# Optimization experiments

Measured on AMD Instinct MI355X. Metric: run time of the kernel, lower is better.

The kernel has to match this reference:

```python
import jax, jax.numpy as jnp
import numpy as np


def _pairwise_sqdist(x, y):
    # x: [B, N, D], y: [B, M, D] -> P: [B, N, M] squared euclidean distances
    xx = jnp.sum(x * x, axis=-1)              # [B, N]
    yy = jnp.sum(y * y, axis=-1)              # [B, M]
    zz = jnp.einsum('bnd,bmd->bnm', x, y)     # [B, N, M]
    return xx[:, :, None] + yy[:, None, :] - 2.0 * zz


def setup_inputs() -> dict:
    key = jax.random.key(0)
    k1, k2 = jax.random.split(key)
    B, N, D = 8, 8192, 3
    preds = jax.random.normal(k1, (B, N, D), dtype=jnp.float32)
    gts = jax.random.normal(k2, (B, N, D), dtype=jnp.float32)
    return {"preds": preds, "gts": gts}


def reference(preds, gts):
    # P = batch_pairwise_dist(gts, preds): P[b, i, j] = ||gts[b,i] - preds[b,j]||^2
    P = _pairwise_sqdist(gts, preds)          # [B, N_gts, N_preds]
    loss_1 = jnp.sum(jnp.min(P, axis=1))      # min over gts points
    loss_2 = jnp.sum(jnp.min(P, axis=2))      # min over pred points
    return loss_1 + loss_2
```

## Files before the change

### kernel.cpp

```cpp
#include <hip/hip_runtime.h>

typedef _Float16 f16;
typedef f16 half8 __attribute__((ext_vector_type(8)));
typedef float f32x16 __attribute__((ext_vector_type(16)));

#define BB 8
#define NN 8192
#define SETPTS (BB * NN)
#define NPTS (2 * SETPTS)
#define TQ NPTS

__device__ __forceinline__ void gload_lds16(const void* g, void* l) {
  __builtin_amdgcn_global_load_lds(
      (const __attribute__((address_space(1))) void*)g,
      (__attribute__((address_space(3))) void*)l, 16, 0, 0);
}

__global__ __launch_bounds__(256) void chamfer_prep(
    const float* __restrict__ preds, const float* __restrict__ gts,
    float* __restrict__ yy, half8* __restrict__ Aq, half8* __restrict__ Bq) {
  int idx = blockIdx.x * 256 + threadIdx.x;
  int s = idx >> 16;
  int off = idx & (SETPTS - 1);
  const float* src = s ? gts : preds;
  float x0 = src[off * 3 + 0], x1 = src[off * 3 + 1], x2 = src[off * 3 + 2];

  f16 h0 = (f16)x0; f16 l0 = (f16)(x0 - (float)h0);
  f16 h1 = (f16)x1; f16 l1 = (f16)(x1 - (float)h1);
  f16 h2 = (f16)x2; f16 l2 = (f16)(x2 - (float)h2);

  float Y0 = -2.f * x0, Y1 = -2.f * x1, Y2 = -2.f * x2;
  f16 H0 = (f16)Y0; f16 L0 = (f16)(Y0 - (float)H0);
  f16 H1 = (f16)Y1; f16 L1 = (f16)(Y1 - (float)H1);
  f16 H2 = (f16)Y2; f16 L2 = (f16)(Y2 - (float)H2);

  float yv = x0 * x0 + x1 * x1 + x2 * x2;
  f16 yh = (f16)yv; f16 yl = (f16)(yv - (float)yh);

  f16 one = (f16)1.f, zz = (f16)0.f;
  half8 A0 = {h0, l0, h0, l0, h1, l1, h1, l1};
  half8 A1 = {h2, l2, h2, l2, one, one, zz, zz};
  half8 B0 = {H0, H0, L0, L0, H1, H1, L1, L1};
  half8 B1 = {H2, H2, L2, L2, yh, yl, zz, zz};

  Aq[idx * 2 + 0] = A0; Aq[idx * 2 + 1] = A1;
  Bq[idx * 2 + 0] = B0; Bq[idx * 2 + 1] = B1;
  yy[idx] = yv;
}

template <int R>
__global__ __launch_bounds__(256, 4) void chamfer_mfma(
    const half8* __restrict__ Aq, const half8* __restrict__ Bq,
    float* __restrict__ partial) {
  constexpr int NSTEP = NN / R / 32;
  constexpr int CH = 16;
  constexpr int NCH = NSTEP / CH;
  __shared__ __align__(16) char lds[2][CH * 1024];

  int bi = blockIdx.x;
  int xcd = bi & 7;
  int idx = bi >> 3;
  int panel = xcd * 2 + (idx & 1);
  int dir = panel >> 3;
  int b = panel & 7;
  int sub = idx >> 1;
  int qb = sub & 31;
  int r = sub >> 5;

  int tid = threadIdx.x;
  int w = tid >> 6;
  int l = tid & 63;
  int l31 = l & 31;
  int lh = l >> 5;

  const half8* Qp =
      Aq + ((size_t)(dir * BB + b) * NN + qb * 256 + w * 64) * 2;
  half8 q0 = Qp[l31 * 2 + lh];
  half8 q1 = Qp[(32 + l31) * 2 + lh];

  const char* gpanel = (const char*)(Bq + ((size_t)((1 - dir) * BB + b) * NN +
                                           r * (NN / R)) * 2);
  int perm = ((l & 31) * 2 + (l >> 5)) * 16;

  auto stage = [&](int buf, int c) {
    const char* csrc = gpanel + (size_t)(c * CH + w * 4) * 1024 + perm;
    char* cdst = &lds[buf][w * 4 * 1024];
#pragma unroll
    for (int i = 0; i < 4; ++i)
      gload_lds16(csrc + i * 1024, cdst + i * 1024);
  };

  f32x16 zero;
#pragma unroll
  for (int i = 0; i < 16; ++i) zero[i] = 0.f;
  float run0 = 3.4e38f, run1 = 3.4e38f;

  stage(0, 0);
  __syncthreads();

#pragma unroll 1
  for (int ch = 0; ch < NCH; ++ch) {
    int par = ch & 1;
    if (ch + 1 < NCH) stage(par ^ 1, ch + 1);
    const half8* lb = (const half8*)&lds[par][0];
#pragma unroll 4
    for (int st = 0; st < CH; ++st) {
      half8 bt = lb[st * 64 + l];
      f32x16 oa = __builtin_amdgcn_mfma_f32_32x32x16_f16(bt, q0, zero, 0, 0, 0);
      f32x16 ob = __builtin_amdgcn_mfma_f32_32x32x16_f16(bt, q1, zero, 0, 0, 0);
      {
        float t0 = fminf(fminf(oa[0], oa[1]), oa[2]);
        float t1 = fminf(fminf(oa[3], oa[4]), oa[5]);
        float t2 = fminf(fminf(oa[6], oa[7]), oa[8]);
        float t3 = fminf(fminf(oa[9], oa[10]), oa[11]);
        float t4 = fminf(fminf(oa[12], oa[13]), oa[14]);
        float u0 = fminf(fminf(t0, t1), t2);
        float u1 = fminf(fminf(t3, t4), oa[15]);
        run0 = fminf(fminf(run0, u0), u1);
      }
      {
        float t0 = fminf(fminf(ob[0], ob[1]), ob[2]);
        float t1 = fminf(fminf(ob[3], ob[4]), ob[5]);
        float t2 = fminf(fminf(ob[6], ob[7]), ob[8]);
        float t3 = fminf(fminf(ob[9], ob[10]), ob[11]);
        float t4 = fminf(fminf(ob[12], ob[13]), ob[14]);
        float u0 = fminf(fminf(t0, t1), t2);
        float u1 = fminf(fminf(t3, t4), ob[15]);
        run1 = fminf(fminf(run1, u0), u1);
      }
    }
    __syncthreads();
  }

  float v0 = fminf(run0, __shfl_xor(run0, 32));
  float v1 = fminf(run1, __shfl_xor(run1, 32));

  size_t qflat = (size_t)(dir * BB + b) * NN + qb * 256 + w * 64;
  float* pr = partial + (size_t)r * TQ + qflat;
  if (lh == 0) {
    pr[l31] = v0;
    pr[32 + l31] = v1;
  }
}

template <int R>
__global__ __launch_bounds__(256) void chamfer_combine(
    const float* __restrict__ partial, const float* __restrict__ yy,
    float* __restrict__ bsums) {
  int q = blockIdx.x * 256 + threadIdx.x;
  float m = partial[q];
#pragma unroll
  for (int rr = 1; rr < R; ++rr) m = fminf(m, partial[(size_t)rr * TQ + q]);
  m += yy[q];
  __shared__ float s[256];
  s[threadIdx.x] = m;
  __syncthreads();
  for (int o = 128; o > 0; o >>= 1) {
    if (threadIdx.x < o) s[threadIdx.x] += s[threadIdx.x + o];
    __syncthreads();
  }
  if (threadIdx.x == 0) bsums[blockIdx.x] = s[0];
}

__global__ __launch_bounds__(256) void chamfer_final(
    const float* __restrict__ bsums, float* __restrict__ out, int n) {
  float v = 0.f;
  for (int i = threadIdx.x; i < n; i += 256) v += bsums[i];
  __shared__ float s[256];
  s[threadIdx.x] = v;
  __syncthreads();
  for (int o = 128; o > 0; o >>= 1) {
    if (threadIdx.x < o) s[threadIdx.x] += s[threadIdx.x + o];
    __syncthreads();
  }
  if (threadIdx.x == 0) out[0] = s[0];
}

extern "C" void kernel_launch(void* const* d_in, const int* in_sizes, int n_in,
                              void* d_out, int out_size, void* d_ws,
                              size_t ws_size, hipStream_t stream) {
  const float* preds = (const float*)d_in[0];
  const float* gts = (const float*)d_in[1];
  float* out = (float*)d_out;

  float* partial = (float*)d_ws;
  float* bsums = partial + (size_t)2 * TQ;
  float* yy = bsums + 1024;
  half8* Aq = (half8*)(yy + NPTS);
  half8* Bq = Aq + (size_t)NPTS * 2;

  chamfer_prep<<<NPTS / 256, 256, 0, stream>>>(preds, gts, yy, Aq, Bq);
  chamfer_mfma<2><<<2 * BB * 32 * 2, 256, 0, stream>>>(Aq, Bq, partial);
  chamfer_combine<2><<<TQ / 256, 256, 0, stream>>>(partial, yy, bsums);
  chamfer_final<<<1, 256, 0, stream>>>(bsums, out, TQ / 256);
}
```

Measured before the change: 46.23 us.

## Widen per-wave query tile to four MFMA blocks and split reference set four ways

Each wave now holds four 32-query fragments instead of two, so every B tile loaded from LDS feeds four MFMAs. This halves LDS reads and staging traffic per unit of compute. The reference panel is split into R=4 slices instead of 2, which keeps the grid at 1024 blocks but doubles the partial-minimum buffer and the combine work. It costs more accumulator registers per thread, which may lower occupancy under the 4-blocks-per-CU launch bound.

```diff
diff --git a/kernel.cpp b/kernel.cpp
--- a/kernel.cpp
+++ b/kernel.cpp
@@ -64,8 +64,8 @@
   int dir = panel >> 3;
   int b = panel & 7;
   int sub = idx >> 1;
-  int qb = sub & 31;
-  int r = sub >> 5;
+  int qb = sub & 15;
+  int r = sub >> 4;
 
   int tid = threadIdx.x;
   int w = tid >> 6;
@@ -74,9 +74,11 @@
   int lh = l >> 5;
 
   const half8* Qp =
-      Aq + ((size_t)(dir * BB + b) * NN + qb * 256 + w * 64) * 2;
-  half8 q0 = Qp[l31 * 2 + lh];
-  half8 q1 = Qp[(32 + l31) * 2 + lh];
+      Aq + ((size_t)(dir * BB + b) * NN + qb * 512 + w * 128) * 2;
+  half8 q0 = Qp[(0 * 32 + l31) * 2 + lh];
+  half8 q1 = Qp[(1 * 32 + l31) * 2 + lh];
+  half8 q2 = Qp[(2 * 32 + l31) * 2 + lh];
+  half8 q3 = Qp[(3 * 32 + l31) * 2 + lh];
 
   const char* gpanel = (const char*)(Bq + ((size_t)((1 - dir) * BB + b) * NN +
                                            r * (NN / R)) * 2);
@@ -93,7 +95,19 @@
   f32x16 zero;
 #pragma unroll
   for (int i = 0; i < 16; ++i) zero[i] = 0.f;
-  float run0 = 3.4e38f, run1 = 3.4e38f;
+  float run0 = 3.4e38f, run1 = 3.4e38f, run2 = 3.4e38f, run3 = 3.4e38f;
+
+#define MINTREE(o, run)                                   \
+  {                                                       \
+    float t0 = fminf(fminf(o[0], o[1]), o[2]);            \
+    float t1 = fminf(fminf(o[3], o[4]), o[5]);            \
+    float t2 = fminf(fminf(o[6], o[7]), o[8]);            \
+    float t3 = fminf(fminf(o[9], o[10]), o[11]);          \
+    float t4 = fminf(fminf(o[12], o[13]), o[14]);         \
+    float u0 = fminf(fminf(t0, t1), t2);                  \
+    float u1 = fminf(fminf(t3, t4), o[15]);               \
+    run = fminf(fminf(run, u0), u1);                      \
+  }
 
   stage(0, 0);
   __syncthreads();
@@ -103,43 +117,34 @@
     int par = ch & 1;
     if (ch + 1 < NCH) stage(par ^ 1, ch + 1);
     const half8* lb = (const half8*)&lds[par][0];
-#pragma unroll 4
+#pragma unroll 2
     for (int st = 0; st < CH; ++st) {
       half8 bt = lb[st * 64 + l];
       f32x16 oa = __builtin_amdgcn_mfma_f32_32x32x16_f16(bt, q0, zero, 0, 0, 0);
       f32x16 ob = __builtin_amdgcn_mfma_f32_32x32x16_f16(bt, q1, zero, 0, 0, 0);
-      {
-        float t0 = fminf(fminf(oa[0], oa[1]), oa[2]);
-        float t1 = fminf(fminf(oa[3], oa[4]), oa[5]);
-        float t2 = fminf(fminf(oa[6], oa[7]), oa[8]);
-        float t3 = fminf(fminf(oa[9], oa[10]), oa[11]);
-        float t4 = fminf(fminf(oa[12], oa[13]), oa[14]);
-        float u0 = fminf(fminf(t0, t1), t2);
-        float u1 = fminf(fminf(t3, t4), oa[15]);
-        run0 = fminf(fminf(run0, u0), u1);
-      }
-      {
-        float t0 = fminf(fminf(ob[0], ob[1]), ob[2]);
-        float t1 = fminf(fminf(ob[3], ob[4]), ob[5]);
-        float t2 = fminf(fminf(ob[6], ob[7]), ob[8]);
-        float t3 = fminf(fminf(ob[9], ob[10]), ob[11]);
-        float t4 = fminf(fminf(ob[12], ob[13]), ob[14]);
-        float u0 = fminf(fminf(t0, t1), t2);
-        float u1 = fminf(fminf(t3, t4), ob[15]);
-        run1 = fminf(fminf(run1, u0), u1);
-      }
+      MINTREE(oa, run0)
+      MINTREE(ob, run1)
+      f32x16 oc = __builtin_amdgcn_mfma_f32_32x32x16_f16(bt, q2, zero, 0, 0, 0);
+      f32x16 od = __builtin_amdgcn_mfma_f32_32x32x16_f16(bt, q3, zero, 0, 0, 0);
+      MINTREE(oc, run2)
+      MINTREE(od, run3)
     }
     __syncthreads();
   }
+#undef MINTREE
 
   float v0 = fminf(run0, __shfl_xor(run0, 32));
   float v1 = fminf(run1, __shfl_xor(run1, 32));
-
-  size_t qflat = (size_t)(dir * BB + b) * NN + qb * 256 + w * 64;
+  float v2 = fminf(run2, __shfl_xor(run2, 32));
+  float v3 = fminf(run3, __shfl_xor(run3, 32));
+
+  size_t qflat = (size_t)(dir * BB + b) * NN + qb * 512 + w * 128;
   float* pr = partial + (size_t)r * TQ + qflat;
   if (lh == 0) {
     pr[l31] = v0;
     pr[32 + l31] = v1;
+    pr[64 + l31] = v2;
+    pr[96 + l31] = v3;
   }
 }
 
@@ -183,14 +188,15 @@
   const float* gts = (const float*)d_in[1];
   float* out = (float*)d_out;
 
+  const int R = 4;
   float* partial = (float*)d_ws;
-  float* bsums = partial + (size_t)2 * TQ;
+  float* bsums = partial + (size_t)R * TQ;
   float* yy = bsums + 1024;
   half8* Aq = (half8*)(yy + NPTS);
   half8* Bq = Aq + (size_t)NPTS * 2;
 
   chamfer_prep<<<NPTS / 256, 256, 0, stream>>>(preds, gts, yy, Aq, Bq);
-  chamfer_mfma<2><<<2 * BB * 32 * 2, 256, 0, stream>>>(Aq, Bq, partial);
-  chamfer_combine<2><<<TQ / 256, 256, 0, stream>>>(partial, yy, bsums);
+  chamfer_mfma<R><<<2 * BB * 16 * R, 256, 0, stream>>>(Aq, Bq, partial);
+  chamfer_combine<R><<<TQ / 256, 256, 0, stream>>>(partial, yy, bsums);
   chamfer_final<<<1, 256, 0, stream>>>(bsums, out, TQ / 256);
 }
```

Result: no change. 45.76 us (-1.0%).
